# Performance work log

Measured on AMD Instinct MI355X. Metric: run time of the kernel, lower is better.

The kernel has to match this reference:

```python
import jax, jax.numpy as jnp
import numpy as np

N_NODES = 50000
N_EDGES = 800000
HEADS = 4
NEG_SLOPE = 0.2  # DGL GATConv default and act1 slope


def _gat_layer(x, src, dst, W, al, ar, b, n_nodes, heads, dh):
    # x: [N, Fin] -> proj: [N, H, Dh]
    proj = (x @ W).reshape(n_nodes, heads, dh)
    el = jnp.einsum('nhd,hd->nh', proj, al)  # [N, H]
    er = jnp.einsum('nhd,hd->nh', proj, ar)  # [N, H]
    e = jax.nn.leaky_relu(el[src] + er[dst], NEG_SLOPE)  # [E, H]
    # segment softmax over incoming edges of each dst node
    m = jax.ops.segment_max(e, dst, num_segments=n_nodes)
    m = jnp.where(jnp.isfinite(m), m, jnp.zeros_like(m))
    ex = jnp.exp(e - m[dst])
    s = jax.ops.segment_sum(ex, dst, num_segments=n_nodes)
    alpha = ex / (s[dst] + 1e-9)  # [E, H]
    msg = proj[src] * alpha[:, :, None]  # [E, H, Dh]
    out = jax.ops.segment_sum(msg, dst, num_segments=n_nodes)  # [N, H, Dh]
    return out.reshape(n_nodes, heads * dh) + b


def setup_inputs() -> dict:
    key = jax.random.key(0)
    ks = jax.random.split(key, 10)
    d = {
        'init_emb': jax.random.normal(ks[0], (N_NODES, 300), jnp.float32) * 0.1,
        'W1': jax.random.normal(ks[1], (300, 400), jnp.float32) * (1.0 / np.sqrt(300)),
        'al1': jax.random.normal(ks[2], (HEADS, 100), jnp.float32) * 0.1,
        'ar1': jax.random.normal(ks[3], (HEADS, 100), jnp.float32) * 0.1,
        'b1': jnp.zeros((400,), jnp.float32),
        'W2': jax.random.normal(ks[4], (400, 512), jnp.float32) * (1.0 / np.sqrt(400)),
        'al2': jax.random.normal(ks[5], (HEADS, 128), jnp.float32) * 0.1,
        'ar2': jax.random.normal(ks[6], (HEADS, 128), jnp.float32) * 0.1,
        'b2': jnp.zeros((512,), jnp.float32),
        'src': jax.random.randint(ks[7], (N_EDGES,), 0, N_NODES, jnp.int32),
        'dst': jax.random.randint(ks[8], (N_EDGES,), 0, N_NODES, jnp.int32),
    }
    return d


def reference(init_emb, W1, al1, ar1, b1, W2, al2, ar2, b2, src, dst):
    x = _gat_layer(init_emb, src, dst, W1, al1, ar1, b1, N_NODES, HEADS, 100)  # [N, 400]
    x = jax.nn.leaky_relu(x, NEG_SLOPE)  # act1
    x = _gat_layer(x, src, dst, W2, al2, ar2, b2, N_NODES, HEADS, 128)  # [N, 512]
    return x
```

## Files before the change

kernel.cpp:

```cpp
#include <hip/hip_runtime.h>
#include <math.h>
#include <stdint.h>

#define NN 50000
#define NE 800000
#define HEADS 4

typedef __attribute__((ext_vector_type(8))) short bf16x8;
typedef __attribute__((ext_vector_type(4))) float f32x4;

__device__ __forceinline__ uint32_t bf16rne(float x) {
  uint32_t b = __float_as_uint(x);
  return (b + 0x7FFFu + ((b >> 16) & 1u)) >> 16;
}
__device__ __forceinline__ float bflo(uint32_t v) {
  return __uint_as_float(v << 16);
}
__device__ __forceinline__ float bfhi(uint32_t v) {
  return __uint_as_float(v & 0xFFFF0000u);
}

__global__ void hist_kernel(const int* __restrict__ dst, int* __restrict__ counts, int n) {
  int i = blockIdx.x * blockDim.x + threadIdx.x;
  if (i < n) atomicAdd(&counts[dst[i]], 1);
}

__global__ void scan_kernel(const int* __restrict__ counts, int* __restrict__ row_ptr, int n) {
  __shared__ int wsum[16];
  const int lane = threadIdx.x & 63;
  const int w = threadIdx.x >> 6;
  int carry = 0;
  for (int start = 0; start < n; start += 1024) {
    int i = start + (int)threadIdx.x;
    int v = (i < n) ? counts[i] : 0;
    int x = v;
#pragma unroll
    for (int off = 1; off < 64; off <<= 1) {
      int t = __shfl_up(x, off);
      if (lane >= off) x += t;
    }
    if (lane == 63) wsum[w] = x;
    __syncthreads();
    if (w == 0 && lane < 16) {
      int s = wsum[lane];
#pragma unroll
      for (int off = 1; off < 16; off <<= 1) {
        int t = __shfl_up(s, off);
        if (lane >= off) s += t;
      }
      wsum[lane] = s;
    }
    __syncthreads();
    int woff = (w > 0) ? wsum[w - 1] : 0;
    int incl = x + woff;
    if (i < n) row_ptr[i] = carry + incl - v;
    carry += wsum[15];
    __syncthreads();
  }
  if (threadIdx.x == 0) row_ptr[n] = carry;
}

__global__ void scatter_kernel(const int* __restrict__ dst, const int* __restrict__ src,
                               const int* __restrict__ row_ptr, int* __restrict__ cursor,
                               int* __restrict__ srcs, int n) {
  int i = blockIdx.x * blockDim.x + threadIdx.x;
  if (i < n) {
    int d = dst[i];
    int pos = atomicAdd(&cursor[d], 1);
    srcs[row_ptr[d] + pos] = src[i];
  }
}

__global__ void build_bt3(const float* __restrict__ B, unsigned short* __restrict__ BT3,
                          int K, int N, int K3p) {
  int kp = blockIdx.x * blockDim.x + threadIdx.x;
  int n = blockIdx.y;
  if (kp >= K3p) return;
  unsigned short out = 0;
  if (n < N && kp < 3 * K) {
    int k = kp / 3;
    int r = kp - 3 * k;
    float v = B[(size_t)k * N + n];
    uint32_t hi = bf16rne(v);
    if (r == 1) {
      float back = __uint_as_float(hi << 16);
      out = (unsigned short)bf16rne(v - back);
    } else {
      out = (unsigned short)hi;
    }
  }
  BT3[(size_t)n * K3p + kp] = out;
}

__global__ __launch_bounds__(256, 2) void gemm_split3(
    const float* __restrict__ A, const unsigned short* __restrict__ BT3,
    unsigned short* __restrict__ Ch, int M, int K, int K3p, int NstR, int RSc,
    int DHR, int DHP, int magic) {
  __shared__ unsigned short As[128 * 96];
  __shared__ unsigned short Bs[128 * 96];
  const int tid = threadIdx.x;
  const int w = tid >> 6, lane = tid & 63;
  const int wr = w >> 1, wc = w & 1;
  const int ln = lane & 15, quad = lane >> 4;
  const int m0 = blockIdx.y * 128, n0 = blockIdx.x * 128;
  const int ar = tid >> 1, ah = tid & 1;
  const long arow = (long)min(m0 + ar, M - 1) * K;

  f32x4 acc[4][4];
#pragma unroll
  for (int mi = 0; mi < 4; ++mi)
#pragma unroll
    for (int ni = 0; ni < 4; ++ni) acc[mi][ni] = (f32x4){0.f, 0.f, 0.f, 0.f};

  const int ksteps = (K + 31) / 32;
  for (int s = 0; s < ksteps; ++s) {
    const int k0 = s * 32;
    const int kp0 = s * 96;
#pragma unroll
    for (int j = 0; j < 6; ++j) {
      int g = (w * 6 + j) * 64 + lane;
      unsigned row = ((unsigned)g * 5462u) >> 16;
      unsigned col = (unsigned)g - row * 12u;
      const unsigned short* gp = BT3 + (size_t)(n0 + row) * K3p + kp0 + col * 8;
      void* lp = (void*)((char*)Bs + (size_t)(w * 6 + j) * 1024);
      __builtin_amdgcn_global_load_lds(
          (const __attribute__((address_space(1))) void*)gp,
          (__attribute__((address_space(3))) void*)lp, 16, 0, 0);
    }
    {
      float f[16];
      const int kb = k0 + ah * 16;
#pragma unroll
      for (int q = 0; q < 4; ++q) {
        int gk = kb + q * 4;
        if (gk + 3 < K) {
          *(float4*)&f[q * 4] = *(const float4*)&A[arow + gk];
        } else {
#pragma unroll
          for (int t = 0; t < 4; ++t) f[q * 4 + t] = (gk + t < K) ? A[arow + gk + t] : 0.f;
        }
      }
      unsigned short tr[48];
#pragma unroll
      for (int j = 0; j < 16; ++j) {
        uint32_t hi = bf16rne(f[j]);
        float back = __uint_as_float(hi << 16);
        uint32_t lo = bf16rne(f[j] - back);
        tr[3 * j + 0] = (unsigned short)hi;
        tr[3 * j + 1] = (unsigned short)hi;
        tr[3 * j + 2] = (unsigned short)lo;
      }
      uint32_t u[24];
#pragma unroll
      for (int i = 0; i < 24; ++i)
        u[i] = (uint32_t)tr[2 * i] | ((uint32_t)tr[2 * i + 1] << 16);
      uint4* dst = (uint4*)((char*)As + ar * 192 + ah * 96);
#pragma unroll
      for (int t = 0; t < 6; ++t) dst[t] = *(uint4*)&u[t * 4];
    }
    __syncthreads();
#pragma unroll
    for (int sub = 0; sub < 3; ++sub) {
      bf16x8 af[4], bfr[4];
#pragma unroll
      for (int mi = 0; mi < 4; ++mi)
        af[mi] = *(const bf16x8*)&As[(wr * 64 + mi * 16 + ln) * 96 + sub * 32 + quad * 8];
#pragma unroll
      for (int ni = 0; ni < 4; ++ni)
        bfr[ni] = *(const bf16x8*)&Bs[(wc * 64 + ni * 16 + ln) * 96 + sub * 32 + quad * 8];
#pragma unroll
      for (int mi = 0; mi < 4; ++mi)
#pragma unroll
        for (int ni = 0; ni < 4; ++ni)
          acc[mi][ni] =
              __builtin_amdgcn_mfma_f32_16x16x32_bf16(af[mi], bfr[ni], acc[mi][ni], 0, 0, 0);
    }
    __syncthreads();
  }
#pragma unroll
  for (int mi = 0; mi < 4; ++mi) {
#pragma unroll
    for (int r = 0; r < 4; ++r) {
      int gm = m0 + wr * 64 + mi * 16 + quad * 4 + r;
      if (gm < M) {
        unsigned short* crow = Ch + (size_t)gm * RSc;
#pragma unroll
        for (int ni = 0; ni < 4; ++ni) {
          int gn = n0 + wc * 64 + ni * 16 + ln;
          if (gn < NstR) {
            int h = (gn * magic) >> 12;
            int col = h * DHP + (gn - h * DHR);
            crow[col] = (unsigned short)bf16rne(acc[mi][ni][r]);
          }
        }
      }
    }
  }
}

template <int DHR, int DHP>
__global__ void el_er_kernel(const unsigned short* __restrict__ projh,
                             const float* __restrict__ al, const float* __restrict__ ar,
                             float* __restrict__ el, float* __restrict__ er) {
  int t = blockIdx.x * blockDim.x + threadIdx.x;
  if (t >= NN * HEADS) return;
  int h = t & (HEADS - 1);
  int n = t >> 2;
  const unsigned short* pr = projh + (size_t)n * (HEADS * DHP) + (size_t)h * DHP;
  const float* alh = al + h * DHR;
  const float* arh = ar + h * DHR;
  float sl = 0.f, sr = 0.f;
#pragma unroll 4
  for (int d = 0; d < DHR; d += 4) {
    uint2 pv = *(const uint2*)&pr[d];
    float p0 = bflo(pv.x), p1 = bfhi(pv.x), p2 = bflo(pv.y), p3 = bfhi(pv.y);
    float4 av = *(const float4*)&alh[d];
    float4 rv = *(const float4*)&arh[d];
    sl += p0 * av.x + p1 * av.y + p2 * av.z + p3 * av.w;
    sr += p0 * rv.x + p1 * rv.y + p2 * rv.z + p3 * rv.w;
  }
  el[t] = sl;
  er[t] = sr;
}

template <int DHP, int DHR, bool ACT>
__global__ __launch_bounds__(256) void aggregate2(
    const unsigned short* __restrict__ projh, const float* __restrict__ el,
    const float* __restrict__ er, const float* __restrict__ bias,
    const int* __restrict__ row_ptr, const int* __restrict__ srcs,
    float* __restrict__ out) {
  constexpr int LPH = DHP / 8;
  constexpr int RS = HEADS * DHP * 2;
  const int node = blockIdx.x * 4 + (threadIdx.x >> 6);
  if (node >= NN) return;
  const int lane = threadIdx.x & 63;
  const int beg = row_ptr[node], end = row_ptr[node + 1];
  const int e16 = lane >> 2, hp = lane & 3;
  const float er_p = er[node * 4 + hp];
  int head;
  if constexpr (LPH == 16) head = lane >> 4;
  else head = (lane * 5) >> 6;
  const int u = lane - head * LPH;
  const int laneByte = head * (DHP * 2) + u * 16;
  const bool active = lane < 4 * LPH;
  const char* pb = (const char*)projh;

  float bv[8];
  const int d0 = u * 8;
#pragma unroll
  for (int j = 0; j < 8; ++j)
    bv[j] = (active && d0 + j < DHR) ? bias[head * DHR + d0 + j] : 0.f;

  float acc[8];
#pragma unroll
  for (int j = 0; j < 8; ++j) acc[j] = 0.f;
  float lsum = 0.f;

  int i = beg;
  for (; i + 16 <= end; i += 16) {
    int sE = srcs[i + e16];
    float ev = el[sE * 4 + hp] + er_p;
    ev = fmaxf(ev, 0.2f * ev);
    float pv_ = __expf(ev);
    int off_ = sE * RS;
#pragma unroll
    for (int e = 0; e < 16; ++e) {
      const int sl = e * 4 + head;
      const float pv = __shfl(pv_, sl);
      const int off = __shfl(off_, sl);
      uint4 q = *(const uint4*)(pb + (uint32_t)(off + laneByte));
      lsum += pv;
      acc[0] += pv * bflo(q.x);
      acc[1] += pv * bfhi(q.x);
      acc[2] += pv * bflo(q.y);
      acc[3] += pv * bfhi(q.y);
      acc[4] += pv * bflo(q.z);
      acc[5] += pv * bfhi(q.z);
      acc[6] += pv * bflo(q.w);
      acc[7] += pv * bfhi(q.w);
    }
  }
  if (i < end) {
    const int rem = end - i;
    int sE = 0;
    float pv_ = 0.f;
    if (e16 < rem) {
      sE = srcs[i + e16];
      float ev = el[sE * 4 + hp] + er_p;
      ev = fmaxf(ev, 0.2f * ev);
      pv_ = __expf(ev);
    }
    int off_ = sE * RS;
#pragma unroll
    for (int e = 0; e < 16; ++e) {
      if (e < rem) {
        const int sl = e * 4 + head;
        const float pv = __shfl(pv_, sl);
        const int off = __shfl(off_, sl);
        uint4 q = *(const uint4*)(pb + (uint32_t)(off + laneByte));
        lsum += pv;
        acc[0] += pv * bflo(q.x);
        acc[1] += pv * bfhi(q.x);
        acc[2] += pv * bflo(q.y);
        acc[3] += pv * bfhi(q.y);
        acc[4] += pv * bflo(q.z);
        acc[5] += pv * bfhi(q.z);
        acc[6] += pv * bflo(q.w);
        acc[7] += pv * bfhi(q.w);
      }
    }
  }

  const float inv = 1.f / (lsum + 1e-9f);
  if (active) {
    float o[8];
#pragma unroll
    for (int j = 0; j < 8; ++j) {
      float v = acc[j] * inv + bv[j];
      if (ACT) v = (v > 0.f) ? v : 0.2f * v;
      o[j] = v;
    }
    float* orow = out + (size_t)node * (HEADS * DHR) + head * DHR + d0;
    *(float4*)orow = make_float4(o[0], o[1], o[2], o[3]);
    if (d0 + 7 < DHR) *(float4*)(orow + 4) = make_float4(o[4], o[5], o[6], o[7]);
  }
}

extern "C" void kernel_launch(void* const* d_in, const int* in_sizes, int n_in,
                              void* d_out, int out_size, void* d_ws, size_t ws_size,
                              hipStream_t stream) {
  const float* init_emb = (const float*)d_in[0];
  const float* W1 = (const float*)d_in[1];
  const float* al1 = (const float*)d_in[2];
  const float* ar1 = (const float*)d_in[3];
  const float* b1 = (const float*)d_in[4];
  const float* W2 = (const float*)d_in[5];
  const float* al2 = (const float*)d_in[6];
  const float* ar2 = (const float*)d_in[7];
  const float* b2 = (const float*)d_in[8];
  const int* src = (const int*)d_in[9];
  const int* dst = (const int*)d_in[10];
  float* out = (float*)d_out;

  char* ws = (char*)d_ws;
  size_t off = 0;
  auto alloc = [&](size_t bytes) {
    void* p = ws + off;
    off += (bytes + 255) & ~((size_t)255);
    return p;
  };
  unsigned short* projh = (unsigned short*)alloc((size_t)NN * 512 * 2);
  float* x1 = (float*)alloc((size_t)NN * 400 * 4);
  float* el = (float*)alloc((size_t)NN * HEADS * 4);
  float* er = (float*)alloc((size_t)NN * HEADS * 4);
  unsigned short* BT3 = (unsigned short*)alloc((size_t)512 * 1248 * 2);
  int* row_ptr = (int*)alloc((size_t)(NN + 1) * 4);
  int* counts = (int*)alloc((size_t)NN * 4);
  int* srcs = (int*)alloc((size_t)NE * 4);

  hipMemsetAsync(counts, 0, (size_t)NN * 4, stream);
  hist_kernel<<<(NE + 255) / 256, 256, 0, stream>>>(dst, counts, NE);
  scan_kernel<<<1, 1024, 0, stream>>>(counts, row_ptr, NN);
  hipMemsetAsync(counts, 0, (size_t)NN * 4, stream);
  scatter_kernel<<<(NE + 255) / 256, 256, 0, stream>>>(dst, src, row_ptr, counts, srcs, NE);

  build_bt3<<<dim3((960 + 255) / 256, 512), 256, 0, stream>>>(W1, BT3, 300, 400, 960);
  gemm_split3<<<dim3(4, (NN + 127) / 128), 256, 0, stream>>>(init_emb, BT3, projh, NN, 300, 960,
                                                             400, 416, 100, 104, 41);
  el_er_kernel<100, 104><<<(NN * HEADS + 255) / 256, 256, 0, stream>>>(projh, al1, ar1, el, er);
  aggregate2<104, 100, true><<<(NN + 3) / 4, 256, 0, stream>>>(projh, el, er, b1, row_ptr, srcs, x1);

  build_bt3<<<dim3((1248 + 255) / 256, 512), 256, 0, stream>>>(W2, BT3, 400, 512, 1248);
  gemm_split3<<<dim3(4, (NN + 127) / 128), 256, 0, stream>>>(x1, BT3, projh, NN, 400, 1248,
                                                             512, 512, 128, 128, 32);
  el_er_kernel<128, 128><<<(NN * HEADS + 255) / 256, 256, 0, stream>>>(projh, al2, ar2, el, er);
  aggregate2<128, 128, false><<<(NN + 3) / 4, 256, 0, stream>>>(projh, el, er, b2, row_ptr, srcs, out);
}
```

Measured before the change: 803.1 us.

## Use persistent warp-per-node aggregation with atomic work queue and prefetched edge scores

Replaces the one-node-per-wavefront grid with a persistent kernel of 2048 blocks in which each wavefront repeatedly claims the next node from a global atomic counter. It also software-pipelines the edge loop by loading the next chunk's source indices and el scores while the current chunk is being accumulated. The aim is to balance the uneven in-degree load across wavefronts, cut launch and tail overhead, and hide the gather latency of srcs/el. In exchange it adds one atomic per node, two extra memsets, and a runtime-bounded remainder loop.

```diff
diff --git a/kernel.cpp b/kernel.cpp
--- a/kernel.cpp
+++ b/kernel.cpp
@@ -224,19 +224,15 @@
 }
 
 template <int DHP, int DHR, bool ACT>
-__global__ __launch_bounds__(256) void aggregate2(
+__global__ __launch_bounds__(256) void aggregate3(
     const unsigned short* __restrict__ projh, const float* __restrict__ el,
     const float* __restrict__ er, const float* __restrict__ bias,
     const int* __restrict__ row_ptr, const int* __restrict__ srcs,
-    float* __restrict__ out) {
+    float* __restrict__ out, int* __restrict__ ctr) {
   constexpr int LPH = DHP / 8;
   constexpr int RS = HEADS * DHP * 2;
-  const int node = blockIdx.x * 4 + (threadIdx.x >> 6);
-  if (node >= NN) return;
   const int lane = threadIdx.x & 63;
-  const int beg = row_ptr[node], end = row_ptr[node + 1];
   const int e16 = lane >> 2, hp = lane & 3;
-  const float er_p = er[node * 4 + hp];
   int head;
   if constexpr (LPH == 16) head = lane >> 4;
   else head = (lane * 5) >> 6;
@@ -251,78 +247,95 @@
   for (int j = 0; j < 8; ++j)
     bv[j] = (active && d0 + j < DHR) ? bias[head * DHR + d0 + j] : 0.f;
 
-  float acc[8];
-#pragma unroll
-  for (int j = 0; j < 8; ++j) acc[j] = 0.f;
-  float lsum = 0.f;
-
-  int i = beg;
-  for (; i + 16 <= end; i += 16) {
-    int sE = srcs[i + e16];
-    float ev = el[sE * 4 + hp] + er_p;
-    ev = fmaxf(ev, 0.2f * ev);
-    float pv_ = __expf(ev);
-    int off_ = sE * RS;
-#pragma unroll
-    for (int e = 0; e < 16; ++e) {
-      const int sl = e * 4 + head;
-      const float pv = __shfl(pv_, sl);
-      const int off = __shfl(off_, sl);
-      uint4 q = *(const uint4*)(pb + (uint32_t)(off + laneByte));
-      lsum += pv;
-      acc[0] += pv * bflo(q.x);
-      acc[1] += pv * bfhi(q.x);
-      acc[2] += pv * bflo(q.y);
-      acc[3] += pv * bfhi(q.y);
-      acc[4] += pv * bflo(q.z);
-      acc[5] += pv * bfhi(q.z);
-      acc[6] += pv * bflo(q.w);
-      acc[7] += pv * bfhi(q.w);
-    }
-  }
-  if (i < end) {
-    const int rem = end - i;
+  for (;;) {
+    int n_;
+    if (lane == 0) n_ = atomicAdd(ctr, 1);
+    const int node = __shfl(n_, 0);
+    if (node >= NN) break;
+
+    const int beg = row_ptr[node], end = row_ptr[node + 1];
+    const float er_p = er[node * 4 + hp];
+
+    float acc[8];
+#pragma unroll
+    for (int j = 0; j < 8; ++j) acc[j] = 0.f;
+    float lsum = 0.f;
+
+    int i = beg;
+    int rem = end - beg;
     int sE = 0;
-    float pv_ = 0.f;
-    if (e16 < rem) {
+    float elv = 0.f;
+    if (rem > 0 && e16 < rem) {
       sE = srcs[i + e16];
-      float ev = el[sE * 4 + hp] + er_p;
+      elv = el[sE * 4 + hp];
+    }
+    while (rem > 0) {
+      const int take = rem < 16 ? rem : 16;
+      float ev = elv + er_p;
       ev = fmaxf(ev, 0.2f * ev);
-      pv_ = __expf(ev);
-    }
-    int off_ = sE * RS;
-#pragma unroll
-    for (int e = 0; e < 16; ++e) {
-      if (e < rem) {
-        const int sl = e * 4 + head;
-        const float pv = __shfl(pv_, sl);
-        const int off = __shfl(off_, sl);
-        uint4 q = *(const uint4*)(pb + (uint32_t)(off + laneByte));
-        lsum += pv;
-        acc[0] += pv * bflo(q.x);
-        acc[1] += pv * bfhi(q.x);
-        acc[2] += pv * bflo(q.y);
-        acc[3] += pv * bfhi(q.y);
-        acc[4] += pv * bflo(q.z);
-        acc[5] += pv * bfhi(q.z);
-        acc[6] += pv * bflo(q.w);
-        acc[7] += pv * bfhi(q.w);
-      }
-    }
-  }
-
-  const float inv = 1.f / (lsum + 1e-9f);
-  if (active) {
-    float o[8];
-#pragma unroll
-    for (int j = 0; j < 8; ++j) {
-      float v = acc[j] * inv + bv[j];
-      if (ACT) v = (v > 0.f) ? v : 0.2f * v;
-      o[j] = v;
-    }
-    float* orow = out + (size_t)node * (HEADS * DHR) + head * DHR + d0;
-    *(float4*)orow = make_float4(o[0], o[1], o[2], o[3]);
-    if (d0 + 7 < DHR) *(float4*)(orow + 4) = make_float4(o[4], o[5], o[6], o[7]);
+      const float pv_ = (e16 < take) ? __expf(ev) : 0.f;
+      const int off_ = sE * RS;
+      const int i2 = i + take;
+      const int rem2 = rem - take;
+      int sEn = 0;
+      float elvn = 0.f;
+      if (rem2 > 0 && e16 < rem2) {
+        sEn = srcs[i2 + e16];
+        elvn = el[sEn * 4 + hp];
+      }
+      if (take == 16) {
+#pragma unroll
+        for (int e = 0; e < 16; ++e) {
+          const int sl = e * 4 + head;
+          const float pv = __shfl(pv_, sl);
+          const int off = __shfl(off_, sl);
+          uint4 q = *(const uint4*)(pb + (uint32_t)(off + laneByte));
+          lsum += pv;
+          acc[0] += pv * bflo(q.x);
+          acc[1] += pv * bfhi(q.x);
+          acc[2] += pv * bflo(q.y);
+          acc[3] += pv * bfhi(q.y);
+          acc[4] += pv * bflo(q.z);
+          acc[5] += pv * bfhi(q.z);
+          acc[6] += pv * bflo(q.w);
+          acc[7] += pv * bfhi(q.w);
+        }
+      } else {
+        for (int e = 0; e < take; ++e) {
+          const int sl = e * 4 + head;
+          const float pv = __shfl(pv_, sl);
+          const int off = __shfl(off_, sl);
+          uint4 q = *(const uint4*)(pb + (uint32_t)(off + laneByte));
+          lsum += pv;
+          acc[0] += pv * bflo(q.x);
+          acc[1] += pv * bfhi(q.x);
+          acc[2] += pv * bflo(q.y);
+          acc[3] += pv * bfhi(q.y);
+          acc[4] += pv * bflo(q.z);
+          acc[5] += pv * bfhi(q.z);
+          acc[6] += pv * bflo(q.w);
+          acc[7] += pv * bfhi(q.w);
+        }
+      }
+      sE = sEn;
+      elv = elvn;
+      i = i2;
+      rem = rem2;
+    }
+
+    const float inv = 1.f / (lsum + 1e-9f);
+    if (active) {
+      float o[8];
+#pragma unroll
+      for (int j = 0; j < 8; ++j) {
+        float v = acc[j] * inv + bv[j];
+        if (ACT) v = (v > 0.f) ? v : 0.2f * v;
+        o[j] = v;
+      }
+      float* orow = out + (size_t)node * (HEADS * DHR) + head * DHR + d0;
+      *(float4*)orow = make_float4(o[0], o[1], o[2], o[3]);
+      if (d0 + 7 < DHR) *(float4*)(orow + 4) = make_float4(o[4], o[5], o[6], o[7]);
+    }
   }
 }
 
@@ -357,6 +370,7 @@
   int* row_ptr = (int*)alloc((size_t)(NN + 1) * 4);
   int* counts = (int*)alloc((size_t)NN * 4);
   int* srcs = (int*)alloc((size_t)NE * 4);
+  int* ctr = (int*)alloc(256);
 
   hipMemsetAsync(counts, 0, (size_t)NN * 4, stream);
   hist_kernel<<<(NE + 255) / 256, 256, 0, stream>>>(dst, counts, NE);
@@ -368,11 +382,13 @@
   gemm_split3<<<dim3(4, (NN + 127) / 128), 256, 0, stream>>>(init_emb, BT3, projh, NN, 300, 960,
                                                              400, 416, 100, 104, 41);
   el_er_kernel<100, 104><<<(NN * HEADS + 255) / 256, 256, 0, stream>>>(projh, al1, ar1, el, er);
-  aggregate2<104, 100, true><<<(NN + 3) / 4, 256, 0, stream>>>(projh, el, er, b1, row_ptr, srcs, x1);
+  hipMemsetAsync(ctr, 0, 4, stream);
+  aggregate3<104, 100, true><<<2048, 256, 0, stream>>>(projh, el, er, b1, row_ptr, srcs, x1, ctr);
 
   build_bt3<<<dim3((1248 + 255) / 256, 512), 256, 0, stream>>>(W2, BT3, 400, 512, 1248);
   gemm_split3<<<dim3(4, (NN + 127) / 128), 256, 0, stream>>>(x1, BT3, projh, NN, 400, 1248,
                                                              512, 512, 128, 128, 32);
   el_er_kernel<128, 128><<<(NN * HEADS + 255) / 256, 256, 0, stream>>>(projh, al2, ar2, el, er);
-  aggregate2<128, 128, false><<<(NN + 3) / 4, 256, 0, stream>>>(projh, el, er, b2, row_ptr, srcs, out);
-}
+  hipMemsetAsync(ctr, 0, 4, stream);
+  aggregate3<128, 128, false><<<2048, 256, 0, stream>>>(projh, el, er, b2, row_ptr, srcs, out, ctr);
+}
```

Measured after the change: 1.901 ms. 137% more time.
